# Optimization experiments

Measured on AMD Instinct MI355X. Metric: run time of the kernel, lower is better.

## Reference

```python
import jax, jax.numpy as jnp
import numpy as np

B, T, D, H = 2, 2048, 1024, 16
DH = D // H  # 64


def setup_inputs() -> dict:
    key = jax.random.key(0)
    ks = jax.random.split(key, 6)
    s = 1.0 / np.sqrt(D)
    return {
        "x": jax.random.normal(ks[0], (B, T, D), dtype=jnp.float32),
        "Wq": jax.random.normal(ks[1], (D, D), dtype=jnp.float32) * s,
        "Wk": jax.random.normal(ks[2], (D, D), dtype=jnp.float32) * s,
        "Wv": jax.random.normal(ks[3], (D, D), dtype=jnp.float32) * s,
        "Wo": jax.random.normal(ks[4], (D, D), dtype=jnp.float32) * s,
        "bo": jnp.zeros((D,), dtype=jnp.float32),
    }


def reference(x, Wq, Wk, Wv, Wo, bo):
    b, t, _ = x.shape
    # projections (torch Linear: x @ W.T; here W stored as [d_in, d_out])
    q = (x @ Wq).reshape(b, t, H, DH).transpose(0, 2, 1, 3)  # [b,H,t,dh]
    k = (x @ Wk).reshape(b, t, H, DH).transpose(0, 2, 1, 3)
    v = (x @ Wv).reshape(b, t, H, DH).transpose(0, 2, 1, 3)
    scores = jnp.einsum("bhqd,bhkd->bhqk", q, k) / np.sqrt(DH).astype(np.float32)
    causal = jnp.tril(jnp.ones((t, t), dtype=bool))  # True = keep
    scores = jnp.where(causal, scores, -jnp.inf)
    weights = jax.nn.softmax(scores, axis=-1)
    ctx = jnp.einsum("bhqk,bhkd->bhqd", weights, v)
    ctx = ctx.transpose(0, 2, 1, 3).reshape(b, t, D)
    return ctx @ Wo + bo
```

## Files before the change

### kernel.cpp

```cpp
#include <hip/hip_runtime.h>


typedef unsigned short u16;
typedef __attribute__((ext_vector_type(8))) short short8;
typedef __attribute__((ext_vector_type(4))) short short4_t;
typedef __attribute__((ext_vector_type(4))) float f32x4;

#define B_ 2
#define T_ 2048
#define D_ 1024
#define H_ 16
#define DH_ 64
#define M_ (B_ * T_)
#define SCALE_LOG2E 0.18033688011112042f
#define NEG_BIG -3.0e4f

#define SLOT_F 4160
#define SLOTS_PER_BH 72
#define OPART_BYTES ((size_t)32 * SLOTS_PER_BH * SLOT_F * 4)
#define WS_BASE_BYTES ((size_t)24 * 1024 * 1024 * 2)

#define GLOAD16(g, l)                                                     \
  __builtin_amdgcn_global_load_lds(                                       \
      (const __attribute__((address_space(1))) void*)(g),                 \
      (__attribute__((address_space(3))) void*)(l), 16, 0, 0)

__device__ __forceinline__ u16 f2bf(float f) {
  union { float f; unsigned u; } v; v.f = f;
  unsigned r = v.u + 0x7fffu + ((v.u >> 16) & 1u);
  return (u16)(r >> 16);
}
__device__ __forceinline__ u16 f2bf_trunc(float f) {
  union { float f; unsigned u; } v; v.f = f;
  return (u16)(v.u >> 16);
}
__device__ __forceinline__ float exp2_raw(float x) {
  float r;
  asm volatile("v_exp_f32 %0, %1" : "=v"(r) : "v"(x));
  return r;
}

__global__ __launch_bounds__(256) void prep(
    const float* __restrict__ x, const float* __restrict__ w0,
    const float* __restrict__ w1, const float* __restrict__ w2,
    const float* __restrict__ w3, u16* __restrict__ xb,
    u16* __restrict__ outT) {
  __shared__ u16 Tl[64][72];
  const int id = blockIdx.x;
  const int tid = threadIdx.x;

  if (id < 2048) {
    const int i = (id * 256 + tid) * 8;
    float4 a = *(const float4*)(x + i);
    float4 b = *(const float4*)(x + i + 4);
    short8 o;
    o[0] = (short)f2bf(a.x); o[1] = (short)f2bf(a.y);
    o[2] = (short)f2bf(a.z); o[3] = (short)f2bf(a.w);
    o[4] = (short)f2bf(b.x); o[5] = (short)f2bf(b.y);
    o[6] = (short)f2bf(b.z); o[7] = (short)f2bf(b.w);
    *(short8*)(xb + i) = o;
    return;
  }

  const int id2 = id - 2048;
  const int z = id2 >> 8;
  const int rem = id2 & 255;
  const int r0 = (rem >> 4) * 64, c0 = (rem & 15) * 64;
  const float* src = (z == 0) ? w0 : (z == 1) ? w1 : (z == 2) ? w2 : w3;
  const int rr = tid >> 2, cc = (tid & 3) * 16;

  const float* p = src + (size_t)(r0 + rr) * D_ + c0 + cc;
  float4 f0 = *(const float4*)p;
  float4 f1 = *(const float4*)(p + 4);
  float4 f2 = *(const float4*)(p + 8);
  float4 f3 = *(const float4*)(p + 12);
  Tl[rr][cc + 0] = f2bf(f0.x); Tl[rr][cc + 1] = f2bf(f0.y);
  Tl[rr][cc + 2] = f2bf(f0.z); Tl[rr][cc + 3] = f2bf(f0.w);
  Tl[rr][cc + 4] = f2bf(f1.x); Tl[rr][cc + 5] = f2bf(f1.y);
  Tl[rr][cc + 6] = f2bf(f1.z); Tl[rr][cc + 7] = f2bf(f1.w);
  Tl[rr][cc + 8] = f2bf(f2.x); Tl[rr][cc + 9] = f2bf(f2.y);
  Tl[rr][cc +10] = f2bf(f2.z); Tl[rr][cc +11] = f2bf(f2.w);
  Tl[rr][cc +12] = f2bf(f3.x); Tl[rr][cc +13] = f2bf(f3.y);
  Tl[rr][cc +14] = f2bf(f3.z); Tl[rr][cc +15] = f2bf(f3.w);
  __syncthreads();

  u16* o = outT + (size_t)z * D_ * D_ + (size_t)(c0 + rr) * D_ + r0 + cc;
  short8 x0, x1;
#pragma unroll
  for (int i = 0; i < 8; i++) x0[i] = (short)Tl[cc + i][rr];
#pragma unroll
  for (int i = 0; i < 8; i++) x1[i] = (short)Tl[cc + 8 + i][rr];
  *(short8*)o = x0;
  *(short8*)(o + 8) = x1;
}

__global__ __launch_bounds__(256) void qkv_gemm(
    const u16* __restrict__ x, const u16* __restrict__ wT,
    u16* __restrict__ qkv) {
  __shared__ u16 As[2][128][32];
  __shared__ u16 Bs[2][128][32];

  const int flat = blockIdx.y * 24 + blockIdx.x;
  const int swz  = (flat & 7) * 96 + (flat >> 3);
  const int n0 = (swz % 24) * 128;
  const int m0 = (swz / 24) * 128;
  const int z = n0 >> 10;
  const int tid = threadIdx.x;
  const int lane = tid & 63, w = tid >> 6;
  const int quad = lane >> 4, l16 = lane & 15;
  const int wr = w >> 1, wc = w & 1;

  f32x4 acc[4][4] = {};
  const int grow = w * 16 + (lane >> 2);
  const int gcol = (lane & 3) * 8;
  const u16* gAr = x + (size_t)(m0 + grow) * D_ + gcol;
  const u16* gBr = wT + (size_t)(n0 + grow) * D_ + gcol;
  const int woff = w * 512;

  {
    u16* lA = (u16*)As + woff;
    u16* lB = (u16*)Bs + woff;
    GLOAD16(gAr, lA);
    GLOAD16(gAr + (size_t)64 * D_, lA + 2048);
    GLOAD16(gBr, lB);
    GLOAD16(gBr + (size_t)64 * D_, lB + 2048);
  }
  __syncthreads();

  int cur = 0;
  for (int k0 = 0; k0 < D_; k0 += 32) {
    if (k0 + 32 < D_) {
      u16* lA = (u16*)As + (cur ^ 1) * 4096 + woff;
      u16* lB = (u16*)Bs + (cur ^ 1) * 4096 + woff;
      const u16* gA = gAr + k0 + 32;
      const u16* gB = gBr + k0 + 32;
      GLOAD16(gA, lA);
      GLOAD16(gA + (size_t)64 * D_, lA + 2048);
      GLOAD16(gB, lB);
      GLOAD16(gB + (size_t)64 * D_, lB + 2048);
    }

    short8 af[4], bf[4];
#pragma unroll
    for (int i = 0; i < 4; i++)
      af[i] = *(const short8*)&As[cur][wr * 64 + i * 16 + l16][quad * 8];
#pragma unroll
    for (int i = 0; i < 4; i++)
      bf[i] = *(const short8*)&Bs[cur][wc * 64 + i * 16 + l16][quad * 8];
    __builtin_amdgcn_s_setprio(1);
#pragma unroll
    for (int i = 0; i < 4; i++)
#pragma unroll
      for (int j = 0; j < 4; j++)
        acc[i][j] = __builtin_amdgcn_mfma_f32_16x16x32_bf16(af[i], bf[j], acc[i][j], 0, 0, 0);
    __builtin_amdgcn_s_setprio(0);

    __syncthreads();
    cur ^= 1;
  }

  if (z < 2) {
    u16* out = qkv + (size_t)z * M_ * D_;
    const float osc = (z == 0) ? SCALE_LOG2E : 1.0f;
#pragma unroll
    for (int i = 0; i < 4; i++) {
#pragma unroll
      for (int j = 0; j < 4; j++) {
        const int n = n0 + wc * 64 + j * 16 + l16;
        const int h = (n >> 6) & 15, dh = n & 63;
#pragma unroll
        for (int r = 0; r < 4; r++) {
          const int m = m0 + wr * 64 + i * 16 + quad * 4 + r;
          const int b = m >> 11, t = m & (T_ - 1);
          out[(((size_t)(b * H_ + h)) * T_ + t) * DH_ + dh] = f2bf(acc[i][j][r] * osc);
        }
      }
    }
  } else {
    u16* vt = qkv + (size_t)2 * M_ * D_;
#pragma unroll
    for (int i = 0; i < 4; i++) {
      const int mm = m0 + wr * 64 + i * 16 + quad * 4;
      const int b = mm >> 11, t = mm & (T_ - 1);
#pragma unroll
      for (int j = 0; j < 4; j++) {
        const int n = n0 + wc * 64 + j * 16 + l16;
        const int h = (n >> 6) & 15, dh = n & 63;
        short4_t pk;
#pragma unroll
        for (int r = 0; r < 4; r++) pk[r] = (short)f2bf(acc[i][j][r]);
        *(short4_t*)(vt + ((size_t)(b * H_ + h) * DH_ + dh) * T_ + t) = pk;
      }
    }
  }
}

__device__ __forceinline__ int slot_base(int qt) {
  return (qt < 16) ? (qt - 8) * 2
       : (qt < 24) ? 16 + (qt - 16) * 3
                   : 40 + (qt - 24) * 4;
}

__global__ __launch_bounds__(128) void attn_chunk(
    const u16* __restrict__ qg, const u16* __restrict__ kg,
    const u16* __restrict__ vtg, u16* __restrict__ ctx,
    float* __restrict__ Opart) {
  __shared__ u16 Ks[64][72];
  __shared__ u16 Vs[64][72];
  __shared__ u16 Ps[2][2][16][72];

  const int cid = 79 - blockIdx.x;
  int qt, c, nc;
  if (cid < 8)       { qt = cid;                    c = 0;               nc = 1; }
  else if (cid < 24) { qt = 8  + ((cid - 8) >> 1);  c = (cid - 8) & 1;   nc = 2; }
  else if (cid < 48) { qt = 16 + (cid - 24) / 3;    c = (cid - 24) % 3;  nc = 3; }
  else               { qt = 24 + ((cid - 48) >> 2); c = (cid - 48) & 3;  nc = 4; }
  const int nt = qt + 1;
  const int kv_lo = (c * nt / nc) * 64;
  const int kv_hi = ((c + 1) * nt / nc) * 64;
  const int q0 = qt * 64;

  const int bh = blockIdx.y;
  const int tid = threadIdx.x;
  const int w = tid >> 6, lane = tid & 63;
  const int quad = lane >> 4, l16 = lane & 15;
  const size_t baseQK = (size_t)bh * T_ * DH_;
  const size_t baseV  = (size_t)bh * DH_ * T_;

  const int qrowA = q0 + w * 32 + l16;
  const int qrowB = qrowA + 16;
  short8 qfA0 = *(const short8*)(qg + baseQK + (size_t)qrowA * DH_ + quad * 8);
  short8 qfA1 = *(const short8*)(qg + baseQK + (size_t)qrowA * DH_ + 32 + quad * 8);
  short8 qfB0 = *(const short8*)(qg + baseQK + (size_t)qrowB * DH_ + quad * 8);
  short8 qfB1 = *(const short8*)(qg + baseQK + (size_t)qrowB * DH_ + 32 + quad * 8);

  f32x4 oaccA[4] = {}, oaccB[4] = {};
  float liA = 0.f, liB = 0.f;

  const int srow = tid >> 1;
  const int scol = (tid & 1) * 32;

  const u16* kp = kg + baseQK + (size_t)(kv_lo + srow) * DH_ + scol;
  const u16* vp = vtg + baseV + (size_t)srow * T_ + kv_lo + scol;
  short8 kr0 = *(const short8*)kp;
  short8 kr1 = *(const short8*)(kp + 8);
  short8 kr2 = *(const short8*)(kp + 16);
  short8 kr3 = *(const short8*)(kp + 24);
  short8 vr0 = *(const short8*)vp;
  short8 vr1 = *(const short8*)(vp + 8);
  short8 vr2 = *(const short8*)(vp + 16);
  short8 vr3 = *(const short8*)(vp + 24);

  for (int kv0 = kv_lo; kv0 < kv_hi; kv0 += 64) {
    __syncthreads();
    *(short8*)&Ks[srow][scol]      = kr0;
    *(short8*)&Ks[srow][scol + 8]  = kr1;
    *(short8*)&Ks[srow][scol + 16] = kr2;
    *(short8*)&Ks[srow][scol + 24] = kr3;
    *(short8*)&Vs[srow][scol]      = vr0;
    *(short8*)&Vs[srow][scol + 8]  = vr1;
    *(short8*)&Vs[srow][scol + 16] = vr2;
    *(short8*)&Vs[srow][scol + 24] = vr3;
    __syncthreads();

    if (kv0 + 64 < kv_hi) {
      const u16* kn = kg + baseQK + (size_t)(kv0 + 64 + srow) * DH_ + scol;
      const u16* vn = vtg + baseV + (size_t)srow * T_ + kv0 + 64 + scol;
      kr0 = *(const short8*)kn;
      kr1 = *(const short8*)(kn + 8);
      kr2 = *(const short8*)(kn + 16);
      kr3 = *(const short8*)(kn + 24);
      vr0 = *(const short8*)vn;
      vr1 = *(const short8*)(vn + 8);
      vr2 = *(const short8*)(vn + 16);
      vr3 = *(const short8*)(vn + 24);
    }

    short8 kf0[4], kf1[4];
#pragma unroll
    for (int cb = 0; cb < 4; cb++) {
      kf0[cb] = *(const short8*)&Ks[cb * 16 + l16][quad * 8];
      kf1[cb] = *(const short8*)&Ks[cb * 16 + l16][32 + quad * 8];
    }

    f32x4 svA[4], svB[4];
    __builtin_amdgcn_s_setprio(1);
#pragma unroll
    for (int cb = 0; cb < 4; cb++) {
      f32x4 z = {};
      svA[cb] = __builtin_amdgcn_mfma_f32_16x16x32_bf16(kf0[cb], qfA0, z, 0, 0, 0);
      svA[cb] = __builtin_amdgcn_mfma_f32_16x16x32_bf16(kf1[cb], qfA1, svA[cb], 0, 0, 0);
      svB[cb] = __builtin_amdgcn_mfma_f32_16x16x32_bf16(kf0[cb], qfB0, z, 0, 0, 0);
      svB[cb] = __builtin_amdgcn_mfma_f32_16x16x32_bf16(kf1[cb], qfB1, svB[cb], 0, 0, 0);
    }
    __builtin_amdgcn_s_setprio(0);

    float pA[4][4], pB[4][4];
    if (kv0 == q0) {
#pragma unroll
      for (int cb = 0; cb < 4; cb++)
#pragma unroll
        for (int r = 0; r < 4; r++) {
          const int kv = kv0 + cb * 16 + quad * 4 + r;
          pA[cb][r] = exp2_raw((kv <= qrowA) ? svA[cb][r] : NEG_BIG);
          pB[cb][r] = exp2_raw((kv <= qrowB) ? svB[cb][r] : NEG_BIG);
        }
    } else {
#pragma unroll
      for (int cb = 0; cb < 4; cb++)
#pragma unroll
        for (int r = 0; r < 4; r++) {
          pA[cb][r] = exp2_raw(svA[cb][r]);
          pB[cb][r] = exp2_raw(svB[cb][r]);
        }
    }
#pragma unroll
    for (int cb = 0; cb < 4; cb++)
#pragma unroll
      for (int r = 0; r < 4; r++) { liA += pA[cb][r]; liB += pB[cb][r]; }

    short8 vf0[4], vf1[4];
#pragma unroll
    for (int cb = 0; cb < 4; cb++) {
      vf0[cb] = *(const short8*)&Vs[cb * 16 + l16][quad * 8];
      vf1[cb] = *(const short8*)&Vs[cb * 16 + l16][32 + quad * 8];
    }

#pragma unroll
    for (int cb = 0; cb < 4; cb++) {
      short4_t pkA, pkB;
#pragma unroll
      for (int r = 0; r < 4; r++) {
        pkA[r] = (short)f2bf_trunc(pA[cb][r]);
        pkB[r] = (short)f2bf_trunc(pB[cb][r]);
      }
      *(short4_t*)&Ps[w][0][l16][cb * 16 + quad * 4] = pkA;
      *(short4_t*)&Ps[w][1][l16][cb * 16 + quad * 4] = pkB;
    }
    short8 paA0 = *(const short8*)&Ps[w][0][l16][quad * 8];
    short8 paA1 = *(const short8*)&Ps[w][0][l16][32 + quad * 8];
    short8 paB0 = *(const short8*)&Ps[w][1][l16][quad * 8];
    short8 paB1 = *(const short8*)&Ps[w][1][l16][32 + quad * 8];
    __builtin_amdgcn_s_setprio(1);
#pragma unroll
    for (int cb = 0; cb < 4; cb++) {
      oaccA[cb] = __builtin_amdgcn_mfma_f32_16x16x32_bf16(vf0[cb], paA0, oaccA[cb], 0, 0, 0);
      oaccA[cb] = __builtin_amdgcn_mfma_f32_16x16x32_bf16(vf1[cb], paA1, oaccA[cb], 0, 0, 0);
      oaccB[cb] = __builtin_amdgcn_mfma_f32_16x16x32_bf16(vf0[cb], paB0, oaccB[cb], 0, 0, 0);
      oaccB[cb] = __builtin_amdgcn_mfma_f32_16x16x32_bf16(vf1[cb], paB1, oaccB[cb], 0, 0, 0);
    }
    __builtin_amdgcn_s_setprio(0);
  }

  liA += __shfl_xor(liA, 16, 64); liA += __shfl_xor(liA, 32, 64);
  liB += __shfl_xor(liB, 16, 64); liB += __shfl_xor(liB, 32, 64);

  if (nc == 1) {
    const int b = bh >> 4, h = bh & 15;
    const float invA = 1.0f / liA, invB = 1.0f / liB;
    u16* outA = ctx + ((size_t)(b * T_ + qrowA)) * D_ + h * 64 + quad * 4;
    u16* outB = ctx + ((size_t)(b * T_ + qrowB)) * D_ + h * 64 + quad * 4;
#pragma unroll
    for (int cb = 0; cb < 4; cb++) {
      short4_t oA, oB;
#pragma unroll
      for (int r = 0; r < 4; r++) {
        oA[r] = (short)f2bf(oaccA[cb][r] * invA);
        oB[r] = (short)f2bf(oaccB[cb][r] * invB);
      }
      *(short4_t*)(outA + cb * 16) = oA;
      *(short4_t*)(outB + cb * 16) = oB;
    }
  } else {
    float* slot = Opart + ((size_t)bh * SLOTS_PER_BH + slot_base(qt) + c) * SLOT_F;
    float* pA = slot + (size_t)(w * 32 + l16) * 64 + quad * 4;
    float* pB = slot + (size_t)(w * 32 + 16 + l16) * 64 + quad * 4;
#pragma unroll
    for (int cb = 0; cb < 4; cb++) {
      *(f32x4*)(pA + cb * 16) = oaccA[cb];
      *(f32x4*)(pB + cb * 16) = oaccB[cb];
    }
    if (quad == 0) {
      slot[4096 + w * 32 + l16] = liA;
      slot[4096 + w * 32 + 16 + l16] = liB;
    }
  }
}

__global__ __launch_bounds__(256) void attn_combine(
    const float* __restrict__ Opart, u16* __restrict__ ctx) {
  __shared__ float ls[64];
  const int qt = blockIdx.x + 8;
  const int bh = blockIdx.y;
  const int nc = 1 + (qt >> 3);
  const float* slot0 = Opart + ((size_t)bh * SLOTS_PER_BH + slot_base(qt)) * SLOT_F;
  const int tid = threadIdx.x;

  if (tid < 64) {
    float s = 0.f;
    for (int c = 0; c < nc; c++) s += slot0[(size_t)c * SLOT_F + 4096 + tid];
    ls[tid] = 1.0f / s;
  }
  __syncthreads();

  const int q = tid >> 2, d0 = (tid & 3) * 16;
  const float* p = slot0 + (size_t)q * 64 + d0;
  f32x4 a0 = *(const f32x4*)(p);
  f32x4 a1 = *(const f32x4*)(p + 4);
  f32x4 a2 = *(const f32x4*)(p + 8);
  f32x4 a3 = *(const f32x4*)(p + 12);
  for (int c = 1; c < nc; c++) {
    const float* pc = p + (size_t)c * SLOT_F;
    a0 += *(const f32x4*)(pc);
    a1 += *(const f32x4*)(pc + 4);
    a2 += *(const f32x4*)(pc + 8);
    a3 += *(const f32x4*)(pc + 12);
  }
  const float inv = ls[q];
  short8 o0, o1;
#pragma unroll
  for (int i = 0; i < 4; i++) {
    o0[i]     = (short)f2bf(a0[i] * inv);
    o0[i + 4] = (short)f2bf(a1[i] * inv);
    o1[i]     = (short)f2bf(a2[i] * inv);
    o1[i + 4] = (short)f2bf(a3[i] * inv);
  }
  const int b = bh >> 4, h = bh & 15;
  u16* op = ctx + ((size_t)(b * T_ + qt * 64 + q)) * D_ + h * 64 + d0;
  *(short8*)op = o0;
  *(short8*)(op + 8) = o1;
}

__global__ __launch_bounds__(128) void attn_mono(
    const u16* __restrict__ qg, const u16* __restrict__ kg,
    const u16* __restrict__ vtg, u16* __restrict__ ctx) {
  __shared__ u16 Ks[64][72];
  __shared__ u16 Vs[64][72];
  __shared__ u16 Ps[2][2][16][72];

  const int qt = gridDim.x - 1 - blockIdx.x;
  const int bh = blockIdx.y;
  const int tid = threadIdx.x;
  const int w = tid >> 6, lane = tid & 63;
  const int quad = lane >> 4, l16 = lane & 15;
  const int q0 = qt * 64;
  const size_t baseQK = (size_t)bh * T_ * DH_;
  const size_t baseV  = (size_t)bh * DH_ * T_;

  const int qrowA = q0 + w * 32 + l16;
  const int qrowB = qrowA + 16;
  short8 qfA0 = *(const short8*)(qg + baseQK + (size_t)qrowA * DH_ + quad * 8);
  short8 qfA1 = *(const short8*)(qg + baseQK + (size_t)qrowA * DH_ + 32 + quad * 8);
  short8 qfB0 = *(const short8*)(qg + baseQK + (size_t)qrowB * DH_ + quad * 8);
  short8 qfB1 = *(const short8*)(qg + baseQK + (size_t)qrowB * DH_ + 32 + quad * 8);

  f32x4 oaccA[4] = {}, oaccB[4] = {};
  float liA = 0.f, liB = 0.f;

  const int srow = tid >> 1;
  const int scol = (tid & 1) * 32;

  const u16* kp = kg + baseQK + (size_t)srow * DH_ + scol;
  const u16* vp = vtg + baseV + (size_t)srow * T_ + scol;
  short8 kr0 = *(const short8*)kp;
  short8 kr1 = *(const short8*)(kp + 8);
  short8 kr2 = *(const short8*)(kp + 16);
  short8 kr3 = *(const short8*)(kp + 24);
  short8 vr0 = *(const short8*)vp;
  short8 vr1 = *(const short8*)(vp + 8);
  short8 vr2 = *(const short8*)(vp + 16);
  short8 vr3 = *(const short8*)(vp + 24);

  for (int kv0 = 0; kv0 <= q0; kv0 += 64) {
    __syncthreads();
    *(short8*)&Ks[srow][scol]      = kr0;
    *(short8*)&Ks[srow][scol + 8]  = kr1;
    *(short8*)&Ks[srow][scol + 16] = kr2;
    *(short8*)&Ks[srow][scol + 24] = kr3;
    *(short8*)&Vs[srow][scol]      = vr0;
    *(short8*)&Vs[srow][scol + 8]  = vr1;
    *(short8*)&Vs[srow][scol + 16] = vr2;
    *(short8*)&Vs[srow][scol + 24] = vr3;
    __syncthreads();
    if (kv0 < q0) {
      const u16* kn = kg + baseQK + (size_t)(kv0 + 64 + srow) * DH_ + scol;
      const u16* vn = vtg + baseV + (size_t)srow * T_ + kv0 + 64 + scol;
      kr0 = *(const short8*)kn;
      kr1 = *(const short8*)(kn + 8);
      kr2 = *(const short8*)(kn + 16);
      kr3 = *(const short8*)(kn + 24);
      vr0 = *(const short8*)vn;
      vr1 = *(const short8*)(vn + 8);
      vr2 = *(const short8*)(vn + 16);
      vr3 = *(const short8*)(vn + 24);
    }

    short8 kf0[4], kf1[4];
#pragma unroll
    for (int cb = 0; cb < 4; cb++) {
      kf0[cb] = *(const short8*)&Ks[cb * 16 + l16][quad * 8];
      kf1[cb] = *(const short8*)&Ks[cb * 16 + l16][32 + quad * 8];
    }

    f32x4 svA[4], svB[4];
#pragma unroll
    for (int cb = 0; cb < 4; cb++) {
      f32x4 z = {};
      svA[cb] = __builtin_amdgcn_mfma_f32_16x16x32_bf16(kf0[cb], qfA0, z, 0, 0, 0);
      svA[cb] = __builtin_amdgcn_mfma_f32_16x16x32_bf16(kf1[cb], qfA1, svA[cb], 0, 0, 0);
      svB[cb] = __builtin_amdgcn_mfma_f32_16x16x32_bf16(kf0[cb], qfB0, z, 0, 0, 0);
      svB[cb] = __builtin_amdgcn_mfma_f32_16x16x32_bf16(kf1[cb], qfB1, svB[cb], 0, 0, 0);
    }

    float pA[4][4], pB[4][4];
    if (kv0 == q0) {
#pragma unroll
      for (int cb = 0; cb < 4; cb++)
#pragma unroll
        for (int r = 0; r < 4; r++) {
          const int kv = kv0 + cb * 16 + quad * 4 + r;
          pA[cb][r] = exp2_raw((kv <= qrowA) ? svA[cb][r] : NEG_BIG);
          pB[cb][r] = exp2_raw((kv <= qrowB) ? svB[cb][r] : NEG_BIG);
        }
    } else {
#pragma unroll
      for (int cb = 0; cb < 4; cb++)
#pragma unroll
        for (int r = 0; r < 4; r++) {
          pA[cb][r] = exp2_raw(svA[cb][r]);
          pB[cb][r] = exp2_raw(svB[cb][r]);
        }
    }
#pragma unroll
    for (int cb = 0; cb < 4; cb++)
#pragma unroll
      for (int r = 0; r < 4; r++) { liA += pA[cb][r]; liB += pB[cb][r]; }

    short8 vf0[4], vf1[4];
#pragma unroll
    for (int cb = 0; cb < 4; cb++) {
      vf0[cb] = *(const short8*)&Vs[cb * 16 + l16][quad * 8];
      vf1[cb] = *(const short8*)&Vs[cb * 16 + l16][32 + quad * 8];
    }

#pragma unroll
    for (int cb = 0; cb < 4; cb++) {
      short4_t pkA, pkB;
#pragma unroll
      for (int r = 0; r < 4; r++) {
        pkA[r] = (short)f2bf_trunc(pA[cb][r]);
        pkB[r] = (short)f2bf_trunc(pB[cb][r]);
      }
      *(short4_t*)&Ps[w][0][l16][cb * 16 + quad * 4] = pkA;
      *(short4_t*)&Ps[w][1][l16][cb * 16 + quad * 4] = pkB;
    }
    short8 paA0 = *(const short8*)&Ps[w][0][l16][quad * 8];
    short8 paA1 = *(const short8*)&Ps[w][0][l16][32 + quad * 8];
    short8 paB0 = *(const short8*)&Ps[w][1][l16][quad * 8];
    short8 paB1 = *(const short8*)&Ps[w][1][l16][32 + quad * 8];
#pragma unroll
    for (int cb = 0; cb < 4; cb++) {
      oaccA[cb] = __builtin_amdgcn_mfma_f32_16x16x32_bf16(vf0[cb], paA0, oaccA[cb], 0, 0, 0);
      oaccA[cb] = __builtin_amdgcn_mfma_f32_16x16x32_bf16(vf1[cb], paA1, oaccA[cb], 0, 0, 0);
      oaccB[cb] = __builtin_amdgcn_mfma_f32_16x16x32_bf16(vf0[cb], paB0, oaccB[cb], 0, 0, 0);
      oaccB[cb] = __builtin_amdgcn_mfma_f32_16x16x32_bf16(vf1[cb], paB1, oaccB[cb], 0, 0, 0);
    }
  }

  liA += __shfl_xor(liA, 16, 64); liA += __shfl_xor(liA, 32, 64);
  liB += __shfl_xor(liB, 16, 64); liB += __shfl_xor(liB, 32, 64);
  const int b = bh >> 4, h = bh & 15;
  const float invA = 1.0f / liA, invB = 1.0f / liB;
  u16* outA = ctx + ((size_t)(b * T_ + qrowA)) * D_ + h * 64 + quad * 4;
  u16* outB = ctx + ((size_t)(b * T_ + qrowB)) * D_ + h * 64 + quad * 4;
#pragma unroll
  for (int cb = 0; cb < 4; cb++) {
    short4_t oA, oB;
#pragma unroll
    for (int r = 0; r < 4; r++) {
      oA[r] = (short)f2bf(oaccA[cb][r] * invA);
      oB[r] = (short)f2bf(oaccB[cb][r] * invB);
    }
    *(short4_t*)(outA + cb * 16) = oA;
    *(short4_t*)(outB + cb * 16) = oB;
  }
}

__global__ __launch_bounds__(256) void out_gemm(
    const u16* __restrict__ ctx, const u16* __restrict__ woT,
    const float* __restrict__ bo, float* __restrict__ out) {
  __shared__ u16 As[2][64][32];
  __shared__ u16 Bs[2][128][32];

  const int flat = blockIdx.y * 8 + blockIdx.x;
  const int swz  = (flat & 7) * 64 + (flat >> 3);
  const int n0 = (swz % 8) * 128;
  const int m0 = (swz / 8) * 64;
  const int tid = threadIdx.x;
  const int lane = tid & 63, w = tid >> 6;
  const int quad = lane >> 4, l16 = lane & 15;
  const int wr = w >> 1, wc = w & 1;

  f32x4 acc[2][4] = {};
  const int grow = w * 16 + (lane >> 2);
  const int gcol = (lane & 3) * 8;
  const u16* gAr = ctx + (size_t)(m0 + grow) * D_ + gcol;
  const u16* gBr = woT + (size_t)(n0 + grow) * D_ + gcol;
  const int woff = w * 512;

  {
    u16* lA = (u16*)As + woff;
    u16* lB = (u16*)Bs + woff;
    GLOAD16(gAr, lA);
    GLOAD16(gBr, lB);
    GLOAD16(gBr + (size_t)64 * D_, lB + 2048);
  }
  __syncthreads();

  int cur = 0;
  for (int k0 = 0; k0 < D_; k0 += 32) {
    if (k0 + 32 < D_) {
      u16* lA = (u16*)As + (cur ^ 1) * 2048 + woff;
      u16* lB = (u16*)Bs + (cur ^ 1) * 4096 + woff;
      const u16* gA = gAr + k0 + 32;
      const u16* gB = gBr + k0 + 32;
      GLOAD16(gA, lA);
      GLOAD16(gB, lB);
      GLOAD16(gB + (size_t)64 * D_, lB + 2048);
    }

    short8 af[2], bf[4];
#pragma unroll
    for (int i = 0; i < 2; i++)
      af[i] = *(const short8*)&As[cur][wr * 32 + i * 16 + l16][quad * 8];
#pragma unroll
    for (int i = 0; i < 4; i++)
      bf[i] = *(const short8*)&Bs[cur][wc * 64 + i * 16 + l16][quad * 8];
    __builtin_amdgcn_s_setprio(1);
#pragma unroll
    for (int i = 0; i < 2; i++)
#pragma unroll
      for (int j = 0; j < 4; j++)
        acc[i][j] = __builtin_amdgcn_mfma_f32_16x16x32_bf16(af[i], bf[j], acc[i][j], 0, 0, 0);
    __builtin_amdgcn_s_setprio(0);

    __syncthreads();
    cur ^= 1;
  }

#pragma unroll
  for (int i = 0; i < 2; i++) {
#pragma unroll
    for (int j = 0; j < 4; j++) {
      const int n = n0 + wc * 64 + j * 16 + l16;
      const float bias = bo[n];
#pragma unroll
      for (int r = 0; r < 4; r++) {
        const int m = m0 + wr * 32 + i * 16 + quad * 4 + r;
        out[(size_t)m * D_ + n] = acc[i][j][r] + bias;
      }
    }
  }
}

extern "C" void kernel_launch(void* const* d_in, const int* in_sizes, int n_in,
                              void* d_out, int out_size, void* d_ws, size_t ws_size,
                              hipStream_t stream) {
  const float* x  = (const float*)d_in[0];
  const float* Wq = (const float*)d_in[1];
  const float* Wk = (const float*)d_in[2];
  const float* Wv = (const float*)d_in[3];
  const float* Wo = (const float*)d_in[4];
  const float* bo = (const float*)d_in[5];
  float* out = (float*)d_out;

  u16* ws  = (u16*)d_ws;
  u16* xb  = ws;
  u16* wT  = xb + (size_t)M_ * D_;
  u16* qkv = wT + (size_t)4 * D_ * D_;
  u16* ctx = qkv + (size_t)3 * M_ * D_;
  u16* vT  = qkv + (size_t)2 * M_ * D_;
  float* Opart = (float*)(ctx + (size_t)M_ * D_);

  prep<<<dim3(3072), 256, 0, stream>>>(x, Wq, Wk, Wv, Wo, xb, wT);
  qkv_gemm<<<dim3(24, 32), 256, 0, stream>>>(xb, wT, qkv);

  if (ws_size >= WS_BASE_BYTES + OPART_BYTES) {
    attn_chunk<<<dim3(80, B_ * H_), 128, 0, stream>>>(
        qkv, qkv + (size_t)M_ * D_, vT, ctx, Opart);
    attn_combine<<<dim3(24, B_ * H_), 256, 0, stream>>>(Opart, ctx);
  } else {
    attn_mono<<<dim3(T_ / 64, B_ * H_), 128, 0, stream>>>(
        qkv, qkv + (size_t)M_ * D_, vT, ctx);
  }

  out_gemm<<<dim3(8, 64), 256, 0, stream>>>(ctx, wT + (size_t)3 * D_ * D_, bo, out);
}
```

Baseline: 189.7 us.

## Split attention chunk work across four waves with one query tile each

The attention chunk kernel moves from 2 waves, each handling two 16-row query tiles, to 4 waves handling one 16-row tile each. Block size doubles to 256 threads, the cooperative K/V staging is spread over more threads, and the P scratch buffer is reshaped to match. The aim is more wave-level parallelism and lower register pressure per wave, to better hide latency. The cost is that each wave reuses its K/V fragment loads from LDS across fewer query rows, so LDS reads per MFMA rise.

```diff
diff --git a/kernel.cpp b/kernel.cpp
--- a/kernel.cpp
+++ b/kernel.cpp
@@ -201,13 +201,13 @@
                    : 40 + (qt - 24) * 4;
 }
 
-__global__ __launch_bounds__(128) void attn_chunk(
+__global__ __launch_bounds__(256) void attn_chunk(
     const u16* __restrict__ qg, const u16* __restrict__ kg,
     const u16* __restrict__ vtg, u16* __restrict__ ctx,
     float* __restrict__ Opart) {
   __shared__ u16 Ks[64][72];
   __shared__ u16 Vs[64][72];
-  __shared__ u16 Ps[2][2][16][72];
+  __shared__ u16 Ps[4][16][72];
 
   const int cid = 79 - blockIdx.x;
   int qt, c, nc;
@@ -227,40 +227,29 @@
   const size_t baseQK = (size_t)bh * T_ * DH_;
   const size_t baseV  = (size_t)bh * DH_ * T_;
 
-  const int qrowA = q0 + w * 32 + l16;
-  const int qrowB = qrowA + 16;
-  short8 qfA0 = *(const short8*)(qg + baseQK + (size_t)qrowA * DH_ + quad * 8);
-  short8 qfA1 = *(const short8*)(qg + baseQK + (size_t)qrowA * DH_ + 32 + quad * 8);
-  short8 qfB0 = *(const short8*)(qg + baseQK + (size_t)qrowB * DH_ + quad * 8);
-  short8 qfB1 = *(const short8*)(qg + baseQK + (size_t)qrowB * DH_ + 32 + quad * 8);
-
-  f32x4 oaccA[4] = {}, oaccB[4] = {};
-  float liA = 0.f, liB = 0.f;
-
-  const int srow = tid >> 1;
-  const int scol = (tid & 1) * 32;
+  const int qrow = q0 + w * 16 + l16;
+  short8 qf0 = *(const short8*)(qg + baseQK + (size_t)qrow * DH_ + quad * 8);
+  short8 qf1 = *(const short8*)(qg + baseQK + (size_t)qrow * DH_ + 32 + quad * 8);
+
+  f32x4 oacc[4] = {};
+  float li = 0.f;
+
+  const int srow = tid >> 2;
+  const int scol = (tid & 3) * 16;
 
   const u16* kp = kg + baseQK + (size_t)(kv_lo + srow) * DH_ + scol;
   const u16* vp = vtg + baseV + (size_t)srow * T_ + kv_lo + scol;
   short8 kr0 = *(const short8*)kp;
   short8 kr1 = *(const short8*)(kp + 8);
-  short8 kr2 = *(const short8*)(kp + 16);
-  short8 kr3 = *(const short8*)(kp + 24);
   short8 vr0 = *(const short8*)vp;
   short8 vr1 = *(const short8*)(vp + 8);
-  short8 vr2 = *(const short8*)(vp + 16);
-  short8 vr3 = *(const short8*)(vp + 24);
 
   for (int kv0 = kv_lo; kv0 < kv_hi; kv0 += 64) {
     __syncthreads();
-    *(short8*)&Ks[srow][scol]      = kr0;
-    *(short8*)&Ks[srow][scol + 8]  = kr1;
-    *(short8*)&Ks[srow][scol + 16] = kr2;
-    *(short8*)&Ks[srow][scol + 24] = kr3;
-    *(short8*)&Vs[srow][scol]      = vr0;
-    *(short8*)&Vs[srow][scol + 8]  = vr1;
-    *(short8*)&Vs[srow][scol + 16] = vr2;
-    *(short8*)&Vs[srow][scol + 24] = vr3;
+    *(short8*)&Ks[srow][scol]     = kr0;
+    *(short8*)&Ks[srow][scol + 8] = kr1;
+    *(short8*)&Vs[srow][scol]     = vr0;
+    *(short8*)&Vs[srow][scol + 8] = vr1;
     __syncthreads();
 
     if (kv0 + 64 < kv_hi) {
@@ -268,12 +257,8 @@
       const u16* vn = vtg + baseV + (size_t)srow * T_ + kv0 + 64 + scol;
       kr0 = *(const short8*)kn;
       kr1 = *(const short8*)(kn + 8);
-      kr2 = *(const short8*)(kn + 16);
-      kr3 = *(const short8*)(kn + 24);
       vr0 = *(const short8*)vn;
       vr1 = *(const short8*)(vn + 8);
-      vr2 = *(const short8*)(vn + 16);
-      vr3 = *(const short8*)(vn + 24);
     }
 
     short8 kf0[4], kf1[4];
@@ -283,41 +268,36 @@
       kf1[cb] = *(const short8*)&Ks[cb * 16 + l16][32 + quad * 8];
     }
 
-    f32x4 svA[4], svB[4];
+    f32x4 sv[4];
     __builtin_amdgcn_s_setprio(1);
 #pragma unroll
     for (int cb = 0; cb < 4; cb++) {
-      f32x4 z = {};
-      svA[cb] = __builtin_amdgcn_mfma_f32_16x16x32_bf16(kf0[cb], qfA0, z, 0, 0, 0);
-      svA[cb] = __builtin_amdgcn_mfma_f32_16x16x32_bf16(kf1[cb], qfA1, svA[cb], 0, 0, 0);
-      svB[cb] = __builtin_amdgcn_mfma_f32_16x16x32_bf16(kf0[cb], qfB0, z, 0, 0, 0);
-      svB[cb] = __builtin_amdgcn_mfma_f32_16x16x32_bf16(kf1[cb], qfB1, svB[cb], 0, 0, 0);
+      f32x4 zz = {};
+      sv[cb] = __builtin_amdgcn_mfma_f32_16x16x32_bf16(kf0[cb], qf0, zz, 0, 0, 0);
+      sv[cb] = __builtin_amdgcn_mfma_f32_16x16x32_bf16(kf1[cb], qf1, sv[cb], 0, 0, 0);
     }
     __builtin_amdgcn_s_setprio(0);
 
-    float pA[4][4], pB[4][4];
+    float pv[4][4];
     if (kv0 == q0) {
 #pragma unroll
       for (int cb = 0; cb < 4; cb++)
 #pragma unroll
         for (int r = 0; r < 4; r++) {
           const int kv = kv0 + cb * 16 + quad * 4 + r;
-          pA[cb][r] = exp2_raw((kv <= qrowA) ? svA[cb][r] : NEG_BIG);
-          pB[cb][r] = exp2_raw((kv <= qrowB) ? svB[cb][r] : NEG_BIG);
+          pv[cb][r] = exp2_raw((kv <= qrow) ? sv[cb][r] : NEG_BIG);
         }
     } else {
 #pragma unroll
       for (int cb = 0; cb < 4; cb++)
 #pragma unroll
-        for (int r = 0; r < 4; r++) {
-          pA[cb][r] = exp2_raw(svA[cb][r]);
-          pB[cb][r] = exp2_raw(svB[cb][r]);
-        }
+        for (int r = 0; r < 4; r++)
+          pv[cb][r] = exp2_raw(sv[cb][r]);
     }
 #pragma unroll
     for (int cb = 0; cb < 4; cb++)
 #pragma unroll
-      for (int r = 0; r < 4; r++) { liA += pA[cb][r]; liB += pB[cb][r]; }
+      for (int r = 0; r < 4; r++) li += pv[cb][r];
 
     short8 vf0[4], vf1[4];
 #pragma unroll
@@ -328,62 +308,43 @@
 
 #pragma unroll
     for (int cb = 0; cb < 4; cb++) {
-      short4_t pkA, pkB;
-#pragma unroll
-      for (int r = 0; r < 4; r++) {
-        pkA[r] = (short)f2bf_trunc(pA[cb][r]);
-        pkB[r] = (short)f2bf_trunc(pB[cb][r]);
-      }
-      *(short4_t*)&Ps[w][0][l16][cb * 16 + quad * 4] = pkA;
-      *(short4_t*)&Ps[w][1][l16][cb * 16 + quad * 4] = pkB;
-    }
-    short8 paA0 = *(const short8*)&Ps[w][0][l16][quad * 8];
-    short8 paA1 = *(const short8*)&Ps[w][0][l16][32 + quad * 8];
-    short8 paB0 = *(const short8*)&Ps[w][1][l16][quad * 8];
-    short8 paB1 = *(const short8*)&Ps[w][1][l16][32 + quad * 8];
+      short4_t pk;
+#pragma unroll
+      for (int r = 0; r < 4; r++) pk[r] = (short)f2bf_trunc(pv[cb][r]);
+      *(short4_t*)&Ps[w][l16][cb * 16 + quad * 4] = pk;
+    }
+    short8 pa0 = *(const short8*)&Ps[w][l16][quad * 8];
+    short8 pa1 = *(const short8*)&Ps[w][l16][32 + quad * 8];
     __builtin_amdgcn_s_setprio(1);
 #pragma unroll
     for (int cb = 0; cb < 4; cb++) {
-      oaccA[cb] = __builtin_amdgcn_mfma_f32_16x16x32_bf16(vf0[cb], paA0, oaccA[cb], 0, 0, 0);
-      oaccA[cb] = __builtin_amdgcn_mfma_f32_16x16x32_bf16(vf1[cb], paA1, oaccA[cb], 0, 0, 0);
-      oaccB[cb] = __builtin_amdgcn_mfma_f32_16x16x32_bf16(vf0[cb], paB0, oaccB[cb], 0, 0, 0);
-      oaccB[cb] = __builtin_amdgcn_mfma_f32_16x16x32_bf16(vf1[cb], paB1, oaccB[cb], 0, 0, 0);
+      oacc[cb] = __builtin_amdgcn_mfma_f32_16x16x32_bf16(vf0[cb], pa0, oacc[cb], 0, 0, 0);
+      oacc[cb] = __builtin_amdgcn_mfma_f32_16x16x32_bf16(vf1[cb], pa1, oacc[cb], 0, 0, 0);
     }
     __builtin_amdgcn_s_setprio(0);
   }
 
-  liA += __shfl_xor(liA, 16, 64); liA += __shfl_xor(liA, 32, 64);
-  liB += __shfl_xor(liB, 16, 64); liB += __shfl_xor(liB, 32, 64);
+  li += __shfl_xor(li, 16, 64); li += __shfl_xor(li, 32, 64);
 
   if (nc == 1) {
     const int b = bh >> 4, h = bh & 15;
-    const float invA = 1.0f / liA, invB = 1.0f / liB;
-    u16* outA = ctx + ((size_t)(b * T_ + qrowA)) * D_ + h * 64 + quad * 4;
-    u16* outB = ctx + ((size_t)(b * T_ + qrowB)) * D_ + h * 64 + quad * 4;
-#pragma unroll
-    for (int cb = 0; cb < 4; cb++) {
-      short4_t oA, oB;
-#pragma unroll
-      for (int r = 0; r < 4; r++) {
-        oA[r] = (short)f2bf(oaccA[cb][r] * invA);
-        oB[r] = (short)f2bf(oaccB[cb][r] * invB);
-      }
-      *(short4_t*)(outA + cb * 16) = oA;
-      *(short4_t*)(outB + cb * 16) = oB;
+    const float inv = 1.0f / li;
+    u16* outp = ctx + ((size_t)(b * T_ + qrow)) * D_ + h * 64 + quad * 4;
+#pragma unroll
+    for (int cb = 0; cb < 4; cb++) {
+      short4_t o;
+#pragma unroll
+      for (int r = 0; r < 4; r++) o[r] = (short)f2bf(oacc[cb][r] * inv);
+      *(short4_t*)(outp + cb * 16) = o;
     }
   } else {
     float* slot = Opart + ((size_t)bh * SLOTS_PER_BH + slot_base(qt) + c) * SLOT_F;
-    float* pA = slot + (size_t)(w * 32 + l16) * 64 + quad * 4;
-    float* pB = slot + (size_t)(w * 32 + 16 + l16) * 64 + quad * 4;
-#pragma unroll
-    for (int cb = 0; cb < 4; cb++) {
-      *(f32x4*)(pA + cb * 16) = oaccA[cb];
-      *(f32x4*)(pB + cb * 16) = oaccB[cb];
-    }
-    if (quad == 0) {
-      slot[4096 + w * 32 + l16] = liA;
-      slot[4096 + w * 32 + 16 + l16] = liB;
-    }
+    float* pq = slot + (size_t)(w * 16 + l16) * 64 + quad * 4;
+#pragma unroll
+    for (int cb = 0; cb < 4; cb++)
+      *(f32x4*)(pq + cb * 16) = oacc[cb];
+    if (quad == 0)
+      slot[4096 + w * 16 + l16] = li;
   }
 }
 
@@ -686,7 +647,7 @@
   qkv_gemm<<<dim3(24, 32), 256, 0, stream>>>(xb, wT, qkv);
 
   if (ws_size >= WS_BASE_BYTES + OPART_BYTES) {
-    attn_chunk<<<dim3(80, B_ * H_), 128, 0, stream>>>(
+    attn_chunk<<<dim3(80, B_ * H_), 256, 0, stream>>>(
         qkv, qkv + (size_t)M_ * D_, vT, ctx, Opart);
     attn_combine<<<dim3(24, B_ * H_), 256, 0, stream>>>(Opart, ctx);
   } else {
```

Result: no change. 190.5 us (+0.4%).
